# Performance work log

Measured on AMD Instinct MI355X. Metric: run time of the kernel, lower is better.

Reference implementation:

```python
import jax, jax.numpy as jnp
import numpy as np

B, T, HD = 128, 256, 512
N_REAL, N_CAT, N_CLASSES, EMB = 32, 4, 100, 8
COMBINED = N_REAL + N_CAT * EMB  # 64
NEG_SLOPE = 0.1


def setup_inputs() -> dict:
    key = jax.random.key(0)
    ks = jax.random.split(key, 20)
    s = lambda *d: 1.0 / np.sqrt(d[0])
    real = jax.random.normal(ks[0], (B, T, N_REAL), dtype=jnp.float32)
    cats = jax.random.randint(ks[1], (B, T, N_CAT), 0, N_CLASSES).astype(jnp.float32)
    x0 = jnp.concatenate([real, cats], axis=-1)
    u = lambda k, shp, fan: jax.random.uniform(k, shp, jnp.float32, -1.0/np.sqrt(fan), 1.0/np.sqrt(fan))
    return {
        'x0': x0,
        'emb': jax.random.normal(ks[2], (N_CAT, N_CLASSES, EMB), dtype=jnp.float32),
        'W1': u(ks[3], (COMBINED, HD), COMBINED), 'b1': u(ks[4], (HD,), COMBINED),
        'W2': u(ks[5], (HD, HD), HD), 'b2': u(ks[6], (HD,), HD),
        'Wi_f': u(ks[7], (HD, 4 * HD), HD), 'bi_f': u(ks[8], (4 * HD,), HD),
        'Wh_f': u(ks[9], (HD, 4 * HD), HD), 'bh_f': u(ks[10], (4 * HD,), HD),
        'Wi_r': u(ks[11], (HD, 4 * HD), HD), 'bi_r': u(ks[12], (4 * HD,), HD),
        'Wh_r': u(ks[13], (HD, 4 * HD), HD), 'bh_r': u(ks[14], (4 * HD,), HD),
        'W3': u(ks[15], (2 * HD, 1), 2 * HD), 'b3': u(ks[16], (1,), 2 * HD),
    }


def leaky(x):
    return jnp.where(x >= 0, x, NEG_SLOPE * x)


def lstm(x, Wi, bi, Wh, bh):
    # x: [B, T, H] -> hidden states [B, T, H]
    b, t, h = x.shape
    xg = jnp.einsum('bti,ig->btg', x, Wi) + bi + bh  # precompute input contribution
    def step(carry, xg_t):
        hk, ck = carry
        g = xg_t + hk @ Wh  # [B, 4H]
        f, i, a, o = jnp.split(g, 4, axis=-1)
        ck = jax.nn.sigmoid(f) * ck + jax.nn.sigmoid(i) * jnp.tanh(a)
        hk = jax.nn.sigmoid(o) * jnp.tanh(ck)
        return (hk, ck), hk
    init = (jnp.zeros((b, h), x.dtype), jnp.zeros((b, h), x.dtype))
    _, hs = jax.lax.scan(step, init, jnp.swapaxes(xg, 0, 1))
    return jnp.swapaxes(hs, 0, 1)


def reference(x0, emb, W1, b1, W2, b2, Wi_f, bi_f, Wh_f, bh_f, Wi_r, bi_r, Wh_r, bh_r, W3, b3):
    real_part = x0[..., :N_REAL]
    idx = x0[..., N_REAL:N_REAL + N_CAT].astype(jnp.int32)  # [B, T, N_CAT]
    emb_out = emb[jnp.arange(N_CAT), idx]                    # [B, T, N_CAT, EMB]
    emb_out = emb_out.reshape(x0.shape[0], x0.shape[1], -1)
    combined = jnp.concatenate([real_part, emb_out], axis=-1)
    x1 = leaky(combined @ W1 + b1)
    x2 = leaky(x1 @ W2 + b2)
    h_f = lstm(x2, Wi_f, bi_f, Wh_f, bh_f)
    h_r = lstm(jnp.flip(x2, axis=1), Wi_r, bi_r, Wh_r, bh_r)
    x3 = jnp.concatenate([h_f, h_r], axis=-1)
    return x3 @ W3 + b3  # [B, T, 1]
```

## Files before the change

kernel.cpp:

```cpp
#include <hip/hip_runtime.h>
#include <cstddef>

namespace {

constexpr int B  = 128;
constexpr int T  = 256;
constexpr int HD = 512;
constexpr int G  = 2048;
constexpr int TC = 32;
constexpr int XIN = 36;
constexpr int NCHUNK = T / TC;

typedef __attribute__((ext_vector_type(8))) short short8;
typedef __attribute__((ext_vector_type(4))) short short4v;
typedef __attribute__((ext_vector_type(4))) float f32x4;

union U16B { uint4 u; short8 s; };

__device__ __forceinline__ float sigmf(float x) { return 1.0f / (1.0f + expf(-x)); }
__device__ __forceinline__ float leakyf(float x) { return x >= 0.0f ? x : 0.1f * x; }

__device__ __forceinline__ unsigned short f2bf(float v) {
  union { float f; unsigned u; } x; x.f = v;
  unsigned r = x.u + 0x7fffu + ((x.u >> 16) & 1u);
  return (unsigned short)(r >> 16);
}
__device__ __forceinline__ float bf2f(unsigned short b) {
  union { unsigned u; float f; } x; x.u = ((unsigned)b) << 16; return x.f;
}

__global__ void k_prep(const float* __restrict__ src, unsigned short* __restrict__ dh,
                       unsigned short* __restrict__ dl, int K, int N) {
  __shared__ float tile[32][33];
  const int n0 = blockIdx.x * 32, k0 = blockIdx.y * 32;
  for (int i = threadIdx.y; i < 32; i += 8)
    tile[i][threadIdx.x] = src[(size_t)(k0 + i) * N + n0 + threadIdx.x];
  __syncthreads();
  for (int i = threadIdx.y; i < 32; i += 8) {
    const float v = tile[threadIdx.x][i];
    const unsigned short h = f2bf(v);
    const size_t o = (size_t)(n0 + i) * K + k0 + threadIdx.x;
    dh[o] = h;
    dl[o] = f2bf(v - bf2f(h));
  }
}

__global__ void k_prep_pack(const float* __restrict__ Whf, const float* __restrict__ Whr,
                            unsigned short* __restrict__ wpkh, unsigned short* __restrict__ wpkl) {
  const int f = blockIdx.x * 256 + threadIdx.x;
  const int l  = f & 63;
  const int ks = (f >> 6) & 15;
  const int ct = (f >> 10) & 7;
  const int ut = (f >> 13) & 15;
  const int dir = f >> 17;
  const float* src = dir ? Whr : Whf;
  const int L = ct * 16 + (l & 15);
  const int gcol = (L >> 5) * HD + ut * 32 + (L & 31);
  const int k0 = ks * 32 + (l >> 4) * 8;
  short8 hv, lv;
  #pragma unroll
  for (int j = 0; j < 8; ++j) {
    const float v = src[(size_t)(k0 + j) * G + gcol];
    const unsigned short h = f2bf(v);
    hv[j] = (short)h;
    lv[j] = (short)f2bf(v - bf2f(h));
  }
  *(short8*)&wpkh[(size_t)f * 8] = hv;
  *(short8*)&wpkl[(size_t)f * 8] = lv;
}

__global__ void k_bias(const float* __restrict__ bif, const float* __restrict__ bhf,
                       const float* __restrict__ bir, const float* __restrict__ bhr,
                       float* __restrict__ biasI) {
  const int i = blockIdx.x * 256 + threadIdx.x;
  const int d = i >> 11, n = i & 2047;
  biasI[i] = (d ? bir[n] : bif[n]) + (d ? bhr[n] : bhf[n]);
}

__global__ void k_embed_gemm1(const float* __restrict__ x0, const float* __restrict__ emb,
                              const float* __restrict__ W1, const float* __restrict__ b1,
                              unsigned short* __restrict__ x1h, unsigned short* __restrict__ x1l) {
  __shared__ float As[64][65];
  __shared__ float Bs[64][68];
  const int tid = threadIdx.x;
  const int m0 = blockIdx.x * 64, n0 = blockIdx.y * 64;

  for (int i = tid; i < 64 * 64; i += 256) {
    const int m = i >> 6, k = i & 63;
    const size_t row = (size_t)(m0 + m);
    float v;
    if (k < 32) {
      v = x0[row * XIN + k];
    } else {
      const int c = (k - 32) >> 3, e = (k - 32) & 7;
      const int idx = (int)x0[row * XIN + 32 + c];
      v = emb[(size_t)(c * 100 + idx) * 8 + e];
    }
    As[m][k] = v;
  }
  for (int j = 0; j < 4; ++j) {
    const int q = tid + 256 * j;
    const int kk = q >> 4, nq = q & 15;
    *(float4*)&Bs[kk][nq * 4] = *(const float4*)&W1[(size_t)kk * HD + n0 + nq * 4];
  }
  __syncthreads();

  const int ty = tid >> 4, tx = tid & 15;
  float acc[4][4] = {};
  #pragma unroll 8
  for (int k = 0; k < 64; ++k) {
    const float a0 = As[ty * 4 + 0][k], a1 = As[ty * 4 + 1][k];
    const float a2 = As[ty * 4 + 2][k], a3 = As[ty * 4 + 3][k];
    const float4 bv = *(const float4*)&Bs[k][tx * 4];
    acc[0][0] += a0 * bv.x; acc[0][1] += a0 * bv.y; acc[0][2] += a0 * bv.z; acc[0][3] += a0 * bv.w;
    acc[1][0] += a1 * bv.x; acc[1][1] += a1 * bv.y; acc[1][2] += a1 * bv.z; acc[1][3] += a1 * bv.w;
    acc[2][0] += a2 * bv.x; acc[2][1] += a2 * bv.y; acc[2][2] += a2 * bv.z; acc[2][3] += a2 * bv.w;
    acc[3][0] += a3 * bv.x; acc[3][1] += a3 * bv.y; acc[3][2] += a3 * bv.z; acc[3][3] += a3 * bv.w;
  }
  const float4 b4 = *(const float4*)&b1[n0 + tx * 4];
  for (int i = 0; i < 4; ++i) {
    float o[4];
    o[0] = leakyf(acc[i][0] + b4.x);
    o[1] = leakyf(acc[i][1] + b4.y);
    o[2] = leakyf(acc[i][2] + b4.z);
    o[3] = leakyf(acc[i][3] + b4.w);
    short4v hv, lv;
    #pragma unroll
    for (int p = 0; p < 4; ++p) {
      const unsigned short hb = f2bf(o[p]);
      hv[p] = (short)hb;
      lv[p] = (short)f2bf(o[p] - bf2f(hb));
    }
    const size_t off = (size_t)(m0 + ty * 4 + i) * HD + n0 + tx * 4;
    *(short4v*)&x1h[off] = hv;
    *(short4v*)&x1l[off] = lv;
  }
}

template <int MODE>
__global__ __launch_bounds__(512) void k_mm(
    const unsigned short* __restrict__ Ah, const unsigned short* __restrict__ Al,
    const unsigned short* __restrict__ Bh, const unsigned short* __restrict__ Bl,
    const float* __restrict__ bias,
    unsigned short* __restrict__ oh, unsigned short* __restrict__ ol,
    float* __restrict__ of, int c0) {
  __shared__ unsigned short As_h[128 * 40], As_l[128 * 40];
  __shared__ unsigned short Bs_h[128 * 40], Bs_l[128 * 40];
  const int tid = threadIdx.x;
  const int m0 = blockIdx.x * 128, n0 = blockIdx.y * 128;
  const int dir = MODE ? (m0 >> 12) : 0;
  const unsigned short* Bhd = Bh + (size_t)dir * G * HD;
  const unsigned short* Bld = Bl + (size_t)dir * G * HD;

  const int si = tid >> 2, sseg = tid & 3;
  int arow;
  if (MODE) {
    const int r = m0 + si;
    const int tc = (r >> 7) & 31, bb = r & 127;
    const int tg = dir ? (T - 1 - (c0 + tc)) : (c0 + tc);
    arow = bb * T + tg;
  } else {
    arow = m0 + si;
  }
  const int brow = n0 + si;

  const int lane = tid & 63;
  const int c16 = lane & 15, q = lane >> 4;
  const int w = tid >> 6;
  const int mg = w & 3, ng = w >> 2;

  f32x4 acc[2][4] = {};

  for (int k0 = 0; k0 < HD; k0 += 32) {
    __syncthreads();
    *(short8*)&As_h[si * 40 + sseg * 8] = *(const short8*)&Ah[(size_t)arow * HD + k0 + sseg * 8];
    *(short8*)&As_l[si * 40 + sseg * 8] = *(const short8*)&Al[(size_t)arow * HD + k0 + sseg * 8];
    *(short8*)&Bs_h[si * 40 + sseg * 8] = *(const short8*)&Bhd[(size_t)brow * HD + k0 + sseg * 8];
    *(short8*)&Bs_l[si * 40 + sseg * 8] = *(const short8*)&Bld[(size_t)brow * HD + k0 + sseg * 8];
    __syncthreads();

    short8 ah[2], al[2], bh[4], bl[4];
    #pragma unroll
    for (int a = 0; a < 2; ++a) {
      const int rr = (2 * mg + a) * 16 + c16;
      ah[a] = *(const short8*)&As_h[rr * 40 + q * 8];
      al[a] = *(const short8*)&As_l[rr * 40 + q * 8];
    }
    #pragma unroll
    for (int j = 0; j < 4; ++j) {
      const int rr = (4 * ng + j) * 16 + c16;
      bh[j] = *(const short8*)&Bs_h[rr * 40 + q * 8];
      bl[j] = *(const short8*)&Bs_l[rr * 40 + q * 8];
    }
    #pragma unroll
    for (int a = 0; a < 2; ++a)
      #pragma unroll
      for (int j = 0; j < 4; ++j) {
        acc[a][j] = __builtin_amdgcn_mfma_f32_16x16x32_bf16(ah[a], bh[j], acc[a][j], 0, 0, 0);
        acc[a][j] = __builtin_amdgcn_mfma_f32_16x16x32_bf16(ah[a], bl[j], acc[a][j], 0, 0, 0);
        acc[a][j] = __builtin_amdgcn_mfma_f32_16x16x32_bf16(al[a], bh[j], acc[a][j], 0, 0, 0);
      }
  }

  #pragma unroll
  for (int a = 0; a < 2; ++a) {
    #pragma unroll
    for (int j = 0; j < 4; ++j) {
      const int nn = n0 + (4 * ng + j) * 16 + c16;
      const float bv = MODE ? bias[dir * G + nn] : bias[nn];
      #pragma unroll
      for (int r = 0; r < 4; ++r) {
        const int mm = m0 + (2 * mg + a) * 16 + 4 * q + r;
        float v = acc[a][j][r] + bv;
        if (MODE) {
          of[(size_t)mm * G + nn] = v;
        } else {
          v = leakyf(v);
          const unsigned short hb = f2bf(v);
          oh[(size_t)mm * HD + nn] = hb;
          ol[(size_t)mm * HD + nn] = f2bf(v - bf2f(hb));
        }
      }
    }
  }
}

__global__ __launch_bounds__(512, 2) void k_scan(
    const float* __restrict__ xg, const unsigned short* __restrict__ wpkh,
    const unsigned short* __restrict__ wpkl, unsigned int* __restrict__ hpk,
    float* __restrict__ cbuf, float* __restrict__ part,
    const float* __restrict__ W3, int* __restrict__ flags, int c0) {
  __shared__ unsigned int hst[16 * 516];
  __shared__ float gl[128 * 17];
  __shared__ float ysum[16 * 33];

  const int tid = threadIdx.x;
  const int bid = blockIdx.x;
  const int dir = bid >> 7;
  const int ut  = (bid >> 3) & 15;
  const int bt  = bid & 7;
  const int u0 = ut * 32, b0 = bt * 16;
  const int w = tid >> 6, lane = tid & 63;
  const int r16 = lane & 15, q = lane >> 4;

  const unsigned short* wp = wpkh + ((size_t)(((dir * 16 + ut) * 8 + w) * 16) << 9) + lane * 8;
  const unsigned short* wq = wpkl + ((size_t)(((dir * 16 + ut) * 8 + w) * 16) << 9) + lane * 8;
#define LDW(K) const short8 wh##K = *(const short8*)(wp + (K) * 512); \
               const short8 wl##K = *(const short8*)(wq + (K) * 512);
  LDW(0) LDW(1) LDW(2) LDW(3) LDW(4) LDW(5) LDW(6) LDW(7)
  LDW(8) LDW(9) LDW(10) LDW(11) LDW(12) LDW(13) LDW(14) LDW(15)
#undef LDW

  const int b_l = tid >> 5, u2 = tid & 31;
  const int bg = b0 + b_l, jg = u0 + u2;
  const size_t ci = ((size_t)dir * B + bg) * HD + jg;
  float creg = (c0 == 0) ? 0.0f : cbuf[ci];
  const float w3v = W3[dir * HD + jg];
  const int fl_base = dir * 8 + bt;
  const int hb = r16 * 516 + q * 8;

#define KSTEP(K) { \
    const uint4 aa = *(const uint4*)&hst[hb + (K) * 32]; \
    const uint4 bb = *(const uint4*)&hst[hb + (K) * 32 + 4]; \
    U16B hiu, lou; \
    hiu.u.x = __builtin_amdgcn_perm(aa.y, aa.x, 0x07060302u); \
    hiu.u.y = __builtin_amdgcn_perm(aa.w, aa.z, 0x07060302u); \
    hiu.u.z = __builtin_amdgcn_perm(bb.y, bb.x, 0x07060302u); \
    hiu.u.w = __builtin_amdgcn_perm(bb.w, bb.z, 0x07060302u); \
    lou.u.x = __builtin_amdgcn_perm(aa.y, aa.x, 0x05040100u); \
    lou.u.y = __builtin_amdgcn_perm(aa.w, aa.z, 0x05040100u); \
    lou.u.z = __builtin_amdgcn_perm(bb.y, bb.x, 0x05040100u); \
    lou.u.w = __builtin_amdgcn_perm(bb.w, bb.z, 0x05040100u); \
    acc = __builtin_amdgcn_mfma_f32_16x16x32_bf16(wh##K, hiu.s, acc, 0, 0, 0); \
    acc = __builtin_amdgcn_mfma_f32_16x16x32_bf16(wh##K, lou.s, acc, 0, 0, 0); \
    acc = __builtin_amdgcn_mfma_f32_16x16x32_bf16(wl##K, hiu.s, acc, 0, 0, 0); }

  for (int tc = 0; tc < TC; ++tc) {
    const int t = c0 + tc;

    const float* xr = xg + (((size_t)dir * TC + tc) * B + bg) * G;
    const float xgf = xr[jg];
    const float xgi = xr[HD + jg];
    const float xga = xr[2 * HD + jg];
    const float xgo = xr[3 * HD + jg];

    f32x4 acc = {0.0f, 0.0f, 0.0f, 0.0f};
    if (t > 0) {
      if (tc > 0) {
        if (tid == 0) {
          while (__hip_atomic_load(&flags[(tc - 1) * 16 + fl_base], __ATOMIC_RELAXED,
                                   __HIP_MEMORY_SCOPE_AGENT) < 16)
            __builtin_amdgcn_s_sleep(1);
        }
        __syncthreads();
      }
      {
        const unsigned int* hsrc = hpk + ((size_t)((t & 1) * 2 + dir) * B + b0) * HD;
        unsigned int hv[16];
        #pragma unroll
        for (int i = 0; i < 16; ++i)
          hv[i] = __hip_atomic_load(&hsrc[i * HD + tid], __ATOMIC_RELAXED,
                                    __HIP_MEMORY_SCOPE_AGENT);
        #pragma unroll
        for (int i = 0; i < 16; ++i)
          hst[i * 516 + tid] = hv[i];
      }
      __syncthreads();
      KSTEP(0) KSTEP(1) KSTEP(2) KSTEP(3) KSTEP(4) KSTEP(5) KSTEP(6) KSTEP(7)
      KSTEP(8) KSTEP(9) KSTEP(10) KSTEP(11) KSTEP(12) KSTEP(13) KSTEP(14) KSTEP(15)
      __syncthreads();
    }

    gl[(w * 16 + q * 4 + 0) * 17 + r16] = acc[0];
    gl[(w * 16 + q * 4 + 1) * 17 + r16] = acc[1];
    gl[(w * 16 + q * 4 + 2) * 17 + r16] = acc[2];
    gl[(w * 16 + q * 4 + 3) * 17 + r16] = acc[3];
    __syncthreads();

    {
      const float gf = gl[(u2) * 17 + b_l]      + xgf;
      const float gi = gl[(32 + u2) * 17 + b_l] + xgi;
      const float ga = gl[(64 + u2) * 17 + b_l] + xga;
      const float go = gl[(96 + u2) * 17 + b_l] + xgo;
      const float cn = sigmf(gf) * creg + sigmf(gi) * tanhf(ga);
      const float hn = sigmf(go) * tanhf(cn);
      creg = cn;
      const unsigned short hh = f2bf(hn);
      const unsigned int hp = ((unsigned)hh << 16) | (unsigned)f2bf(hn - bf2f(hh));
      __hip_atomic_store(&hpk[((size_t)(((t + 1) & 1) * 2 + dir) * B + bg) * HD + jg], hp,
                         __ATOMIC_RELAXED, __HIP_MEMORY_SCOPE_AGENT);
      ysum[b_l * 33 + u2] = hn * w3v;
    }
    __syncthreads();

    if (tid == 0)
      __hip_atomic_fetch_add(&flags[tc * 16 + fl_base], 1, __ATOMIC_RELAXED,
                             __HIP_MEMORY_SCOPE_AGENT);
    if (tid < 16) {
      float s = 0.0f;
      #pragma unroll
      for (int i = 0; i < 32; ++i) s += ysum[tid * 33 + i];
      part[((size_t)t * 32 + dir * 16 + ut) * B + b0 + tid] = s;
    }
  }
#undef KSTEP

  cbuf[ci] = creg;
}

__global__ void k_out(const float* __restrict__ part, const float* __restrict__ b3,
                      float* __restrict__ out) {
  const int o = blockIdx.x * 256 + threadIdx.x;
  const int b = o & 127, t = o >> 7;
  float s = b3[0];
  #pragma unroll
  for (int g = 0; g < 32; ++g) s += part[((size_t)t * 32 + g) * B + b];
  out[(size_t)b * T + t] = s;
}

}

extern "C" void kernel_launch(void* const* d_in, const int* in_sizes, int n_in,
                              void* d_out, int out_size, void* d_ws, size_t ws_size,
                              hipStream_t stream) {
  const float* x0   = (const float*)d_in[0];
  const float* emb  = (const float*)d_in[1];
  const float* W1   = (const float*)d_in[2];
  const float* b1   = (const float*)d_in[3];
  const float* W2   = (const float*)d_in[4];
  const float* b2   = (const float*)d_in[5];
  const float* Wi_f = (const float*)d_in[6];
  const float* bi_f = (const float*)d_in[7];
  const float* Wh_f = (const float*)d_in[8];
  const float* bh_f = (const float*)d_in[9];
  const float* Wi_r = (const float*)d_in[10];
  const float* bi_r = (const float*)d_in[11];
  const float* Wh_r = (const float*)d_in[12];
  const float* bh_r = (const float*)d_in[13];
  const float* W3   = (const float*)d_in[14];
  const float* b3   = (const float*)d_in[15];
  float* out = (float*)d_out;

  char* wsb = (char*)d_ws;
  unsigned short* x1h  = (unsigned short*)(wsb + 0);
  unsigned short* x1l  = (unsigned short*)(wsb + 33554432);
  float*          xgf  = (float*)(wsb + 0);
  unsigned short* x2h  = (unsigned short*)(wsb + 67108864);
  unsigned short* x2l  = (unsigned short*)(wsb + 100663296);
  unsigned short* wih  = (unsigned short*)(wsb + 134217728);
  unsigned short* wil  = (unsigned short*)(wsb + 138412032);
  unsigned short* w2h  = (unsigned short*)(wsb + 142606336);
  unsigned short* w2l  = (unsigned short*)(wsb + 143130624);
  unsigned short* wpkh = (unsigned short*)(wsb + 143654912);
  unsigned short* wpkl = (unsigned short*)(wsb + 147849216);
  unsigned int*   hpk  = (unsigned int*)(wsb + 152043520);
  float*          cbuf = (float*)(wsb + 153092096);
  float*          part = (float*)(wsb + 153616384);
  float*          bia  = (float*)(wsb + 157810688);
  int*            flg  = (int*)(wsb + 157827072);

  k_prep_pack<<<dim3(1024), 256, 0, stream>>>(Wh_f, Wh_r, wpkh, wpkl);
  k_prep<<<dim3(G / 32, HD / 32), dim3(32, 8), 0, stream>>>(Wi_f, wih, wil, HD, G);
  k_prep<<<dim3(G / 32, HD / 32), dim3(32, 8), 0, stream>>>(Wi_r, wih + (size_t)G * HD, wil + (size_t)G * HD, HD, G);
  k_prep<<<dim3(HD / 32, HD / 32), dim3(32, 8), 0, stream>>>(W2, w2h, w2l, HD, HD);
  k_bias<<<dim3(16), 256, 0, stream>>>(bi_f, bh_f, bi_r, bh_r, bia);

  k_embed_gemm1<<<dim3(B * T / 64, HD / 64), 256, 0, stream>>>(x0, emb, W1, b1, x1h, x1l);

  k_mm<0><<<dim3(B * T / 128, HD / 128), 512, 0, stream>>>(
      x1h, x1l, w2h, w2l, b2, x2h, x2l, nullptr, 0);

  void* args[9];
  int c0 = 0;
  args[0] = (void*)&xgf;  args[1] = (void*)&wpkh; args[2] = (void*)&wpkl;
  args[3] = (void*)&hpk;  args[4] = (void*)&cbuf; args[5] = (void*)&part;
  args[6] = (void*)&W3;   args[7] = (void*)&flg;  args[8] = (void*)&c0;

  for (int c = 0; c < NCHUNK; ++c) {
    c0 = c * TC;
    k_mm<1><<<dim3(2 * TC * B / 128, G / 128), 512, 0, stream>>>(
        x2h, x2l, wih, wil, bia, nullptr, nullptr, xgf, c0);
    hipMemsetAsync(flg, 0, TC * 16 * sizeof(int), stream);
    hipLaunchCooperativeKernel((void*)k_scan, dim3(256), dim3(512), args, 0, stream);
  }

  k_out<<<dim3(B * T / 256), 256, 0, stream>>>(part, b3, out);
}
```

Before: 1.839 ms.

## Fuse next-chunk input GEMM into LSTM scan kernel with double-buffered gates

The input-projection GEMM for the next time chunk now runs inside the cooperative scan kernel, interleaved with the recurrent steps and written to a second gate buffer, so the separate k_mm launch per chunk goes away. The chunk length drops from 32 to 16 steps so the fused GEMM tiles spread evenly across scan iterations. The hidden-state hi/lo split is also moved from the MFMA inner loop to the global-to-LDS load, so each step holds separate hi and lo LDS arrays. The aim is to hide GEMM time behind the latency-bound recurrence, but it adds LDS pressure, extra barriers on the serial path and twice as many scan launches.

```diff
diff --git a/kernel.cpp b/kernel.cpp
--- a/kernel.cpp
+++ b/kernel.cpp
@@ -7,15 +7,13 @@
 constexpr int T  = 256;
 constexpr int HD = 512;
 constexpr int G  = 2048;
-constexpr int TC = 32;
+constexpr int TC = 16;
 constexpr int XIN = 36;
 constexpr int NCHUNK = T / TC;
 
 typedef __attribute__((ext_vector_type(8))) short short8;
 typedef __attribute__((ext_vector_type(4))) short short4v;
 typedef __attribute__((ext_vector_type(4))) float f32x4;
-
-union U16B { uint4 u; short8 s; };
 
 __device__ __forceinline__ float sigmf(float x) { return 1.0f / (1.0f + expf(-x)); }
 __device__ __forceinline__ float leakyf(float x) { return x >= 0.0f ? x : 0.1f * x; }
@@ -148,7 +146,7 @@
   __shared__ unsigned short Bs_h[128 * 40], Bs_l[128 * 40];
   const int tid = threadIdx.x;
   const int m0 = blockIdx.x * 128, n0 = blockIdx.y * 128;
-  const int dir = MODE ? (m0 >> 12) : 0;
+  const int dir = MODE ? (m0 / (TC * B)) : 0;
   const unsigned short* Bhd = Bh + (size_t)dir * G * HD;
   const unsigned short* Bld = Bl + (size_t)dir * G * HD;
 
@@ -156,8 +154,8 @@
   int arow;
   if (MODE) {
     const int r = m0 + si;
-    const int tc = (r >> 7) & 31, bb = r & 127;
-    const int tg = dir ? (T - 1 - (c0 + tc)) : (c0 + tc);
+    const int tcc = (r >> 7) & (TC - 1), bb = r & (B - 1);
+    const int tg = dir ? (T - 1 - (c0 + tcc)) : (c0 + tcc);
     arow = bb * T + tg;
   } else {
     arow = m0 + si;
@@ -226,13 +224,20 @@
 }
 
 __global__ __launch_bounds__(512, 2) void k_scan(
-    const float* __restrict__ xg, const unsigned short* __restrict__ wpkh,
-    const unsigned short* __restrict__ wpkl, unsigned int* __restrict__ hpk,
-    float* __restrict__ cbuf, float* __restrict__ part,
-    const float* __restrict__ W3, int* __restrict__ flags, int c0) {
-  __shared__ unsigned int hst[16 * 516];
+    const float* __restrict__ xg, float* __restrict__ xgn,
+    const unsigned short* __restrict__ wpkh, const unsigned short* __restrict__ wpkl,
+    unsigned int* __restrict__ hpk, float* __restrict__ cbuf,
+    float* __restrict__ part, const float* __restrict__ W3,
+    int* __restrict__ flags, int c0,
+    const unsigned short* __restrict__ x2h, const unsigned short* __restrict__ x2l,
+    const unsigned short* __restrict__ wih, const unsigned short* __restrict__ wil,
+    const float* __restrict__ bia, int do_gemm) {
+  __shared__ unsigned short hsh[16 * 520];
+  __shared__ unsigned short hsl[16 * 520];
   __shared__ float gl[128 * 17];
   __shared__ float ysum[16 * 33];
+  __shared__ unsigned short gAh[128 * 40], gAl[128 * 40];
+  __shared__ unsigned short gBh[128 * 40], gBl[128 * 40];
 
   const int tid = threadIdx.x;
   const int bid = blockIdx.x;
@@ -257,23 +262,21 @@
   float creg = (c0 == 0) ? 0.0f : cbuf[ci];
   const float w3v = W3[dir * HD + jg];
   const int fl_base = dir * 8 + bt;
-  const int hb = r16 * 516 + q * 8;
+  const int lr = tid & 31;
+  unsigned int* hh32 = (unsigned int*)hsh;
+  unsigned int* hl32 = (unsigned int*)hsl;
+
+  const int c0n = c0 + TC;
+  const int mg = w & 3, ng = w >> 2;
+  const int gsi = tid >> 2, gseg = tid & 3;
+  f32x4 gacc[2][4] = {};
 
 #define KSTEP(K) { \
-    const uint4 aa = *(const uint4*)&hst[hb + (K) * 32]; \
-    const uint4 bb = *(const uint4*)&hst[hb + (K) * 32 + 4]; \
-    U16B hiu, lou; \
-    hiu.u.x = __builtin_amdgcn_perm(aa.y, aa.x, 0x07060302u); \
-    hiu.u.y = __builtin_amdgcn_perm(aa.w, aa.z, 0x07060302u); \
-    hiu.u.z = __builtin_amdgcn_perm(bb.y, bb.x, 0x07060302u); \
-    hiu.u.w = __builtin_amdgcn_perm(bb.w, bb.z, 0x07060302u); \
-    lou.u.x = __builtin_amdgcn_perm(aa.y, aa.x, 0x05040100u); \
-    lou.u.y = __builtin_amdgcn_perm(aa.w, aa.z, 0x05040100u); \
-    lou.u.z = __builtin_amdgcn_perm(bb.y, bb.x, 0x05040100u); \
-    lou.u.w = __builtin_amdgcn_perm(bb.w, bb.z, 0x05040100u); \
-    acc = __builtin_amdgcn_mfma_f32_16x16x32_bf16(wh##K, hiu.s, acc, 0, 0, 0); \
-    acc = __builtin_amdgcn_mfma_f32_16x16x32_bf16(wh##K, lou.s, acc, 0, 0, 0); \
-    acc = __builtin_amdgcn_mfma_f32_16x16x32_bf16(wl##K, hiu.s, acc, 0, 0, 0); }
+    const short8 bhv = *(const short8*)&hsh[r16 * 520 + (K) * 32 + q * 8]; \
+    const short8 blv = *(const short8*)&hsl[r16 * 520 + (K) * 32 + q * 8]; \
+    acc = __builtin_amdgcn_mfma_f32_16x16x32_bf16(wh##K, bhv, acc, 0, 0, 0); \
+    acc = __builtin_amdgcn_mfma_f32_16x16x32_bf16(wh##K, blv, acc, 0, 0, 0); \
+    acc = __builtin_amdgcn_mfma_f32_16x16x32_bf16(wl##K, bhv, acc, 0, 0, 0); }
 
   for (int tc = 0; tc < TC; ++tc) {
     const int t = c0 + tc;
@@ -295,15 +298,16 @@
         __syncthreads();
       }
       {
-        const unsigned int* hsrc = hpk + ((size_t)((t & 1) * 2 + dir) * B + b0) * HD;
-        unsigned int hv[16];
+        const unsigned long long* hsrc = (const unsigned long long*)(
+            hpk + ((size_t)((t & 1) * 2 + dir) * B + b0 + b_l) * HD);
         #pragma unroll
-        for (int i = 0; i < 16; ++i)
-          hv[i] = __hip_atomic_load(&hsrc[i * HD + tid], __ATOMIC_RELAXED,
-                                    __HIP_MEMORY_SCOPE_AGENT);
-        #pragma unroll
-        for (int i = 0; i < 16; ++i)
-          hst[i * 516 + tid] = hv[i];
+        for (int p = 0; p < 8; ++p) {
+          const unsigned long long v = __hip_atomic_load(&hsrc[p * 32 + lr], __ATOMIC_RELAXED,
+                                                         __HIP_MEMORY_SCOPE_AGENT);
+          const unsigned int p0 = (unsigned int)v, p1 = (unsigned int)(v >> 32);
+          hh32[b_l * 260 + p * 32 + lr] = __builtin_amdgcn_perm(p1, p0, 0x07060302u);
+          hl32[b_l * 260 + p * 32 + lr] = __builtin_amdgcn_perm(p1, p0, 0x05040100u);
+        }
       }
       __syncthreads();
       KSTEP(0) KSTEP(1) KSTEP(2) KSTEP(3) KSTEP(4) KSTEP(5) KSTEP(6) KSTEP(7)
@@ -325,8 +329,8 @@
       const float cn = sigmf(gf) * creg + sigmf(gi) * tanhf(ga);
       const float hn = sigmf(go) * tanhf(cn);
       creg = cn;
-      const unsigned short hh = f2bf(hn);
-      const unsigned int hp = ((unsigned)hh << 16) | (unsigned)f2bf(hn - bf2f(hh));
+      const unsigned short hh16 = f2bf(hn);
+      const unsigned int hp = ((unsigned)hh16 << 16) | (unsigned)f2bf(hn - bf2f(hh16));
       __hip_atomic_store(&hpk[((size_t)(((t + 1) & 1) * 2 + dir) * B + bg) * HD + jg], hp,
                          __ATOMIC_RELAXED, __HIP_MEMORY_SCOPE_AGENT);
       ysum[b_l * 33 + u2] = hn * w3v;
@@ -341,6 +345,77 @@
       #pragma unroll
       for (int i = 0; i < 32; ++i) s += ysum[tid * 33 + i];
       part[((size_t)t * 32 + dir * 16 + ut) * B + b0 + tid] = s;
+    }
+
+    if (do_gemm) {
+      #pragma unroll
+      for (int rep = 0; rep < 2; ++rep) {
+        const int s = tc * 2 + rep;
+        const int ls = s & 15;
+        const int tt = bid * 2 + (s >> 4);
+        const int m0g = (tt & 31) * 128, n0g = (tt >> 5) * 128;
+        const int dirg = m0g >> 11;
+        const int rr0 = m0g + gsi;
+        const int tcc = (rr0 >> 7) & (TC - 1), bb2 = rr0 & (B - 1);
+        const int tg = dirg ? (T - 1 - (c0n + tcc)) : (c0n + tcc);
+        const int arow = bb2 * T + tg;
+        const int brow = n0g + gsi;
+        const int k0g = ls * 32;
+        const unsigned short* Bhd = wih + (size_t)dirg * G * HD;
+        const unsigned short* Bld = wil + (size_t)dirg * G * HD;
+
+        __syncthreads();
+        *(short8*)&gAh[gsi * 40 + gseg * 8] = *(const short8*)&x2h[(size_t)arow * HD + k0g + gseg * 8];
+        *(short8*)&gAl[gsi * 40 + gseg * 8] = *(const short8*)&x2l[(size_t)arow * HD + k0g + gseg * 8];
+        *(short8*)&gBh[gsi * 40 + gseg * 8] = *(const short8*)&Bhd[(size_t)brow * HD + k0g + gseg * 8];
+        *(short8*)&gBl[gsi * 40 + gseg * 8] = *(const short8*)&Bld[(size_t)brow * HD + k0g + gseg * 8];
+        __syncthreads();
+
+        if (ls == 0) {
+          #pragma unroll
+          for (int a = 0; a < 2; ++a)
+            #pragma unroll
+            for (int j = 0; j < 4; ++j)
+              gacc[a][j] = (f32x4){0.f, 0.f, 0.f, 0.f};
+        }
+
+        short8 ah[2], al[2], bh4[4], bl4[4];
+        #pragma unroll
+        for (int a = 0; a < 2; ++a) {
+          const int rr = (2 * mg + a) * 16 + r16;
+          ah[a] = *(const short8*)&gAh[rr * 40 + q * 8];
+          al[a] = *(const short8*)&gAl[rr * 40 + q * 8];
+        }
+        #pragma unroll
+        for (int j = 0; j < 4; ++j) {
+          const int rr = (4 * ng + j) * 16 + r16;
+          bh4[j] = *(const short8*)&gBh[rr * 40 + q * 8];
+          bl4[j] = *(const short8*)&gBl[rr * 40 + q * 8];
+        }
+        #pragma unroll
+        for (int a = 0; a < 2; ++a)
+          #pragma unroll
+          for (int j = 0; j < 4; ++j) {
+            gacc[a][j] = __builtin_amdgcn_mfma_f32_16x16x32_bf16(ah[a], bh4[j], gacc[a][j], 0, 0, 0);
+            gacc[a][j] = __builtin_amdgcn_mfma_f32_16x16x32_bf16(ah[a], bl4[j], gacc[a][j], 0, 0, 0);
+            gacc[a][j] = __builtin_amdgcn_mfma_f32_16x16x32_bf16(al[a], bh4[j], gacc[a][j], 0, 0, 0);
+          }
+
+        if (ls == 15) {
+          #pragma unroll
+          for (int a = 0; a < 2; ++a)
+            #pragma unroll
+            for (int j = 0; j < 4; ++j) {
+              const int nn = n0g + (4 * ng + j) * 16 + r16;
+              const float bv = bia[dirg * G + nn];
+              #pragma unroll
+              for (int r = 0; r < 4; ++r) {
+                const int mm = m0g + (2 * mg + a) * 16 + 4 * q + r;
+                xgn[(size_t)mm * G + nn] = gacc[a][j][r] + bv;
+              }
+            }
+        }
+      }
     }
   }
 #undef KSTEP
@@ -384,7 +459,8 @@
   char* wsb = (char*)d_ws;
   unsigned short* x1h  = (unsigned short*)(wsb + 0);
   unsigned short* x1l  = (unsigned short*)(wsb + 33554432);
-  float*          xgf  = (float*)(wsb + 0);
+  float*          xgA  = (float*)(wsb + 0);
+  float*          xgB  = (float*)(wsb + 33554432);
   unsigned short* x2h  = (unsigned short*)(wsb + 67108864);
   unsigned short* x2l  = (unsigned short*)(wsb + 100663296);
   unsigned short* wih  = (unsigned short*)(wsb + 134217728);
@@ -410,16 +486,28 @@
   k_mm<0><<<dim3(B * T / 128, HD / 128), 512, 0, stream>>>(
       x1h, x1l, w2h, w2l, b2, x2h, x2l, nullptr, 0);
 
-  void* args[9];
-  int c0 = 0;
-  args[0] = (void*)&xgf;  args[1] = (void*)&wpkh; args[2] = (void*)&wpkl;
-  args[3] = (void*)&hpk;  args[4] = (void*)&cbuf; args[5] = (void*)&part;
-  args[6] = (void*)&W3;   args[7] = (void*)&flg;  args[8] = (void*)&c0;
+  k_mm<1><<<dim3(2 * TC * B / 128, G / 128), 512, 0, stream>>>(
+      x2h, x2l, wih, wil, bia, nullptr, nullptr, xgA, 0);
+
+  float* xgbuf[2] = {xgA, xgB};
+  const float* xg_cur;
+  float* xg_nxt;
+  int c0 = 0, dog = 1;
+  void* args[16];
+  args[0]  = (void*)&xg_cur; args[1]  = (void*)&xg_nxt;
+  args[2]  = (void*)&wpkh;   args[3]  = (void*)&wpkl;
+  args[4]  = (void*)&hpk;    args[5]  = (void*)&cbuf;
+  args[6]  = (void*)&part;   args[7]  = (void*)&W3;
+  args[8]  = (void*)&flg;    args[9]  = (void*)&c0;
+  args[10] = (void*)&x2h;    args[11] = (void*)&x2l;
+  args[12] = (void*)&wih;    args[13] = (void*)&wil;
+  args[14] = (void*)&bia;    args[15] = (void*)&dog;
 
   for (int c = 0; c < NCHUNK; ++c) {
     c0 = c * TC;
-    k_mm<1><<<dim3(2 * TC * B / 128, G / 128), 512, 0, stream>>>(
-        x2h, x2l, wih, wil, bia, nullptr, nullptr, xgf, c0);
+    dog = (c + 1 < NCHUNK) ? 1 : 0;
+    xg_cur = xgbuf[c & 1];
+    xg_nxt = xgbuf[(c + 1) & 1];
     hipMemsetAsync(flg, 0, TC * 16 * sizeof(int), stream);
     hipLaunchCooperativeKernel((void*)k_scan, dim3(256), dim3(512), args, 0, stream);
   }
```

New measurement: 2.636 ms. 1.43x slower.

## Split hidden state into hi/lo bf16 LDS arrays and remap block indices

Applied to the files above, without the earlier changes.

Packed hi/lo hidden values are now unpacked once during the global-to-LDS copy into separate hi and lo bf16 arrays. The MFMA inner loop then loads short8 operands directly, with no per-K-step permute instructions. The copy uses 64-bit atomic loads per thread instead of 32-bit ones. Block-to-(dir, unit tile, batch tile) mapping is also permuted, which changes which blocks share a batch tile and likely their placement across XCDs, and so the locality of flag and h-state traffic.

```diff
diff --git a/kernel.cpp b/kernel.cpp
--- a/kernel.cpp
+++ b/kernel.cpp
@@ -14,8 +14,6 @@
 typedef __attribute__((ext_vector_type(8))) short short8;
 typedef __attribute__((ext_vector_type(4))) short short4v;
 typedef __attribute__((ext_vector_type(4))) float f32x4;
-
-union U16B { uint4 u; short8 s; };
 
 __device__ __forceinline__ float sigmf(float x) { return 1.0f / (1.0f + expf(-x)); }
 __device__ __forceinline__ float leakyf(float x) { return x >= 0.0f ? x : 0.1f * x; }
@@ -230,15 +228,19 @@
     const unsigned short* __restrict__ wpkl, unsigned int* __restrict__ hpk,
     float* __restrict__ cbuf, float* __restrict__ part,
     const float* __restrict__ W3, int* __restrict__ flags, int c0) {
-  __shared__ unsigned int hst[16 * 516];
+  __shared__ unsigned short hsh[16 * 520];
+  __shared__ unsigned short hsl[16 * 520];
   __shared__ float gl[128 * 17];
   __shared__ float ysum[16 * 33];
 
   const int tid = threadIdx.x;
   const int bid = blockIdx.x;
-  const int dir = bid >> 7;
-  const int ut  = (bid >> 3) & 15;
-  const int bt  = bid & 7;
+  const int x8  = bid & 7;
+  const int r8  = bid >> 3;
+  const int bt  = r8 & 7;
+  const int g   = ((r8 >> 3) << 3) + x8;
+  const int dir = g >> 4;
+  const int ut  = g & 15;
   const int u0 = ut * 32, b0 = bt * 16;
   const int w = tid >> 6, lane = tid & 63;
   const int r16 = lane & 15, q = lane >> 4;
@@ -257,23 +259,16 @@
   float creg = (c0 == 0) ? 0.0f : cbuf[ci];
   const float w3v = W3[dir * HD + jg];
   const int fl_base = dir * 8 + bt;
-  const int hb = r16 * 516 + q * 8;
+  const int lr = tid & 31;
+  unsigned int* hh32 = (unsigned int*)hsh;
+  unsigned int* hl32 = (unsigned int*)hsl;
 
 #define KSTEP(K) { \
-    const uint4 aa = *(const uint4*)&hst[hb + (K) * 32]; \
-    const uint4 bb = *(const uint4*)&hst[hb + (K) * 32 + 4]; \
-    U16B hiu, lou; \
-    hiu.u.x = __builtin_amdgcn_perm(aa.y, aa.x, 0x07060302u); \
-    hiu.u.y = __builtin_amdgcn_perm(aa.w, aa.z, 0x07060302u); \
-    hiu.u.z = __builtin_amdgcn_perm(bb.y, bb.x, 0x07060302u); \
-    hiu.u.w = __builtin_amdgcn_perm(bb.w, bb.z, 0x07060302u); \
-    lou.u.x = __builtin_amdgcn_perm(aa.y, aa.x, 0x05040100u); \
-    lou.u.y = __builtin_amdgcn_perm(aa.w, aa.z, 0x05040100u); \
-    lou.u.z = __builtin_amdgcn_perm(bb.y, bb.x, 0x05040100u); \
-    lou.u.w = __builtin_amdgcn_perm(bb.w, bb.z, 0x05040100u); \
-    acc = __builtin_amdgcn_mfma_f32_16x16x32_bf16(wh##K, hiu.s, acc, 0, 0, 0); \
-    acc = __builtin_amdgcn_mfma_f32_16x16x32_bf16(wh##K, lou.s, acc, 0, 0, 0); \
-    acc = __builtin_amdgcn_mfma_f32_16x16x32_bf16(wl##K, hiu.s, acc, 0, 0, 0); }
+    const short8 bhv = *(const short8*)&hsh[r16 * 520 + (K) * 32 + q * 8]; \
+    const short8 blv = *(const short8*)&hsl[r16 * 520 + (K) * 32 + q * 8]; \
+    acc = __builtin_amdgcn_mfma_f32_16x16x32_bf16(wh##K, bhv, acc, 0, 0, 0); \
+    acc = __builtin_amdgcn_mfma_f32_16x16x32_bf16(wh##K, blv, acc, 0, 0, 0); \
+    acc = __builtin_amdgcn_mfma_f32_16x16x32_bf16(wl##K, bhv, acc, 0, 0, 0); }
 
   for (int tc = 0; tc < TC; ++tc) {
     const int t = c0 + tc;
@@ -295,15 +290,16 @@
         __syncthreads();
       }
       {
-        const unsigned int* hsrc = hpk + ((size_t)((t & 1) * 2 + dir) * B + b0) * HD;
-        unsigned int hv[16];
+        const unsigned long long* hsrc = (const unsigned long long*)(
+            hpk + ((size_t)((t & 1) * 2 + dir) * B + b0 + b_l) * HD);
         #pragma unroll
-        for (int i = 0; i < 16; ++i)
-          hv[i] = __hip_atomic_load(&hsrc[i * HD + tid], __ATOMIC_RELAXED,
-                                    __HIP_MEMORY_SCOPE_AGENT);
-        #pragma unroll
-        for (int i = 0; i < 16; ++i)
-          hst[i * 516 + tid] = hv[i];
+        for (int p = 0; p < 8; ++p) {
+          const unsigned long long v = __hip_atomic_load(&hsrc[p * 32 + lr], __ATOMIC_RELAXED,
+                                                         __HIP_MEMORY_SCOPE_AGENT);
+          const unsigned int p0 = (unsigned int)v, p1 = (unsigned int)(v >> 32);
+          hh32[b_l * 260 + p * 32 + lr] = __builtin_amdgcn_perm(p1, p0, 0x07060302u);
+          hl32[b_l * 260 + p * 32 + lr] = __builtin_amdgcn_perm(p1, p0, 0x05040100u);
+        }
       }
       __syncthreads();
       KSTEP(0) KSTEP(1) KSTEP(2) KSTEP(3) KSTEP(4) KSTEP(5) KSTEP(6) KSTEP(7)
@@ -325,8 +321,8 @@
       const float cn = sigmf(gf) * creg + sigmf(gi) * tanhf(ga);
       const float hn = sigmf(go) * tanhf(cn);
       creg = cn;
-      const unsigned short hh = f2bf(hn);
-      const unsigned int hp = ((unsigned)hh << 16) | (unsigned)f2bf(hn - bf2f(hh));
+      const unsigned short hh16 = f2bf(hn);
+      const unsigned int hp = ((unsigned)hh16 << 16) | (unsigned)f2bf(hn - bf2f(hh16));
       __hip_atomic_store(&hpk[((size_t)(((t + 1) & 1) * 2 + dir) * B + bg) * HD + jg], hp,
                          __ATOMIC_RELAXED, __HIP_MEMORY_SCOPE_AGENT);
       ysum[b_l * 33 + u2] = hn * w3v;
```

New measurement: 3.433 ms. 86.7% more time.
